# Kernel tuning notes

Hardware: AMD Instinct MI355X
Metric: run time of the kernel (lower is better)

The kernel has to match this reference:

```python
import jax, jax.numpy as jnp
import numpy as np

NUM_DAYOFWEEK, NUM_TIME, NUM_MONTH, NUM_DAY = 7, 24, 12, 31
NUM_DESTINATION = 100000
NUM_FACTOR = 128
NUM_DIM = NUM_FACTOR // 4  # 32
N = 1048576


def setup_inputs() -> dict:
    key = jax.random.key(0)
    ks = jax.random.split(key, 10)
    std = 0.1
    return {
        "dayofweek": jax.random.randint(ks[0], (N,), 0, NUM_DAYOFWEEK),
        "time": jax.random.randint(ks[1], (N,), 0, NUM_TIME),
        "month": jax.random.randint(ks[2], (N,), 0, NUM_MONTH),
        "day": jax.random.randint(ks[3], (N,), 0, NUM_DAY),
        "destination": jax.random.randint(ks[4], (N,), 0, NUM_DESTINATION),
        "W_dayofweek": std * jax.random.normal(ks[5], (NUM_DAYOFWEEK, NUM_DIM), dtype=jnp.float32),
        "W_time": std * jax.random.normal(ks[6], (NUM_TIME, NUM_DIM), dtype=jnp.float32),
        "W_month": std * jax.random.normal(ks[7], (NUM_MONTH, NUM_DIM), dtype=jnp.float32),
        "W_day": std * jax.random.normal(ks[8], (NUM_DAY, NUM_DIM), dtype=jnp.float32),
        "W_item": std * jax.random.normal(ks[9], (NUM_DESTINATION, NUM_FACTOR), dtype=jnp.float32),
    }


def reference(dayofweek, time, month, day, destination,
              W_dayofweek, W_time, W_month, W_day, W_item) -> jnp.ndarray:
    # Gather per-feature embeddings and concat into user vector [N, num_factor]
    user = jnp.concatenate([
        W_dayofweek[dayofweek],  # [N, 32]
        W_time[time],            # [N, 32]
        W_month[month],          # [N, 32]
        W_day[day],              # [N, 32]
    ], axis=-1)
    item = W_item[destination]   # [N, 128]
    # Original: diagonal(mm(user, item.T)) == rowwise dot product; compute it directly.
    return jnp.sum(user * item, axis=-1)  # [N]
```

## Files before the change

### kernel.cpp

```cpp
#include <hip/hip_runtime.h>


typedef unsigned long long u64;

constexpr int NDIM = 32;
constexpr int SZ_DOW = 7 * NDIM, SZ_TIM = 24 * NDIM, SZ_MON = 12 * NDIM, SZ_DAY = 31 * NDIM;
constexpr int B_DOW = 0;
constexpr int B_TIM = B_DOW + SZ_DOW;
constexpr int B_MON = B_TIM + SZ_TIM;
constexpr int B_DAY = B_MON + SZ_MON;
constexpr int TAB_TOT = B_DAY + SZ_DAY;

constexpr int NB     = 32;
constexpr int DDIV   = 3125;
constexpr int SLICES = 256;
constexpr int SPB    = 4096;
constexpr int BIN_T  = 1024;
constexpr int IPT    = SPB / BIN_T;

__device__ __forceinline__ unsigned short f2bf(float f) {
    const unsigned u = __float_as_uint(f);
    return (unsigned short)((u + 0x7FFFu + ((u >> 16) & 1u)) >> 16);
}

__device__ __forceinline__ float dot8bf(uint4 a, float4 u0, float4 u1) {
    float s;
    s  = __uint_as_float(a.x << 16)          * u0.x;
    s += __uint_as_float(a.x & 0xFFFF0000u)  * u0.y;
    s += __uint_as_float(a.y << 16)          * u0.z;
    s += __uint_as_float(a.y & 0xFFFF0000u)  * u0.w;
    s += __uint_as_float(a.z << 16)          * u1.x;
    s += __uint_as_float(a.z & 0xFFFF0000u)  * u1.y;
    s += __uint_as_float(a.w << 16)          * u1.z;
    s += __uint_as_float(a.w & 0xFFFF0000u)  * u1.w;
    return s;
}

__device__ __forceinline__ void load_tab(float* tab, const float* Wdow, const float* Wtim,
                                         const float* Wmon, const float* Wday, int nthr) {
    const int t = threadIdx.x;
    for (int i = t; i < SZ_DOW; i += nthr) tab[B_DOW + i] = Wdow[i];
    for (int i = t; i < SZ_TIM; i += nthr) tab[B_TIM + i] = Wtim[i];
    for (int i = t; i < SZ_MON; i += nthr) tab[B_MON + i] = Wmon[i];
    for (int i = t; i < SZ_DAY; i += nthr) tab[B_DAY + i] = Wday[i];
}

__global__ __launch_bounds__(BIN_T)
void prep_kernel(const int* __restrict__ dow, const int* __restrict__ tim,
                 const int* __restrict__ mon, const int* __restrict__ day,
                 const int* __restrict__ dest,
                 int* __restrict__ cntG, int* __restrict__ lbaseG,
                 u64* __restrict__ payload, int n,
                 const float* __restrict__ Witem, unsigned short* __restrict__ Wb,
                 int witem_elems)
{
    __shared__ u64 stage[SPB];
    __shared__ int hist[NB], lbase[NB], cursor[NB];

    const int t = threadIdx.x, b = blockIdx.x;
    const int g0 = b * SPB;
    const int rem = n - g0;
    const int len = rem < SPB ? rem : SPB;

    int dreg[IPT], pkreg[IPT];
#pragma unroll
    for (int i = 0; i < IPT; i++) {
        const int k = i * BIN_T + t;
        if (k < len) {
            const int idx = g0 + k;
            dreg[i]  = dest[idx];
            pkreg[i] = dow[idx] | (tim[idx] << 3) | (mon[idx] << 8) | (day[idx] << 12);
        } else { dreg[i] = -1; pkreg[i] = 0; }
    }

    if (Wb) {
        const int nf4   = witem_elems >> 2;
        const int chunk = (nf4 + SLICES - 1) / SLICES;
        const int c0    = b * chunk;
        const int c1    = min(c0 + chunk, nf4);
        const float4* src = (const float4*)Witem;
        ushort4* dst = (ushort4*)Wb;
        for (int i = c0 + t; i < c1; i += BIN_T) {
            const float4 v = src[i];
            ushort4 o;
            o.x = f2bf(v.x); o.y = f2bf(v.y); o.z = f2bf(v.z); o.w = f2bf(v.w);
            dst[i] = o;
        }
    }

    if (t < NB) hist[t] = 0;
    __syncthreads();
#pragma unroll
    for (int i = 0; i < IPT; i++)
        if (dreg[i] >= 0) atomicAdd(&hist[dreg[i] / DDIV], 1);
    __syncthreads();
    if (t == 0) {
        int run = 0;
        for (int q = 0; q < NB; q++) { lbase[q] = run; run += hist[q]; }
    }
    __syncthreads();
    if (t < NB) { cursor[t] = lbase[t]; cntG[b * NB + t] = hist[t]; lbaseG[b * NB + t] = lbase[t]; }
    __syncthreads();
#pragma unroll
    for (int i = 0; i < IPT; i++) {
        const int k = i * BIN_T + t;
        if (k < len) {
            const int j = atomicAdd(&cursor[dreg[i] / DDIV], 1);
            stage[j] = (u64)(unsigned)(g0 + k)
                     | ((u64)(unsigned)dreg[i]  << 20)
                     | ((u64)(unsigned)pkreg[i] << 37);
        }
    }
    __syncthreads();
#pragma unroll
    for (int i = 0; i < IPT; i++) {
        const int k = i * BIN_T + t;
        if (k < len) payload[g0 + k] = stage[k];
    }
}

__global__ __launch_bounds__(256, 8)
void mf_main_bf16(const u64* __restrict__ payload,
                  const float* __restrict__ Wdow, const float* __restrict__ Wtim,
                  const float* __restrict__ Wmon, const float* __restrict__ Wday,
                  const unsigned short* __restrict__ Wb,
                  const int* __restrict__ cntG, const int* __restrict__ lbaseG,
                  float* __restrict__ out)
{
    __shared__ float tab[TAB_TOT];
    load_tab(tab, Wdow, Wtim, Wmon, Wday, 256);
    __syncthreads();

    const int tid = threadIdx.x;
    const int sub = tid & 63;
    const int wv  = tid >> 6;
    const int g   = sub >> 3;
    const int l8  = sub & 7;
    const int jt   = l8 >> 1;
    const int half = (l8 & 1) * 16;
    const int tbj  = (jt == 0) ? B_DOW : (jt == 1) ? B_TIM : (jt == 2) ? B_MON : B_DAY;
    const int shj  = (jt == 0) ? 37    : (jt == 1) ? 40    : (jt == 2) ? 45    : 49;
    const int mkj  = (jt == 0) ? 7     : (jt == 1) ? 31    : (jt == 2) ? 15    : 31;

    const int x = blockIdx.x & 7;
    const int s = blockIdx.x >> 3;

    for (int p = 0; p < 4; p++) {
        const int q  = x + 8 * p;
        const int L  = cntG[s * NB + q];
        const int st = s * SPB + lbaseG[s * NB + q];

        int i = wv * 16;
        u64 p0 = (i + g < L)     ? payload[st + i + g]     : 0ull;
        u64 p1 = (i + 8 + g < L) ? payload[st + i + 8 + g] : 0ull;

        for (; i < L; i += 64) {
            const bool v0 = (i + g) < L, v1 = (i + 8 + g) < L;
            const u64 c0 = p0, c1 = p1;
            const int ni = i + 64;
            p0 = (ni + g < L)     ? payload[st + ni + g]     : 0ull;
            p1 = (ni + 8 + g < L) ? payload[st + ni + 8 + g] : 0ull;

            const int d0 = (int)((c0 >> 20) & 0x1FFFFull);
            const int d1 = (int)((c1 >> 20) & 0x1FFFFull);

            const uint4* r0 = (const uint4*)(Wb + (long)d0 * 128 + (l8 << 4));
            const uint4* r1 = (const uint4*)(Wb + (long)d1 * 128 + (l8 << 4));
            const uint4 A0 = r0[0], B0 = r0[1];
            const uint4 A1 = r1[0], B1 = r1[1];

            const int ix0 = (int)((c0 >> shj) & (u64)mkj);
            const int ix1 = (int)((c1 >> shj) & (u64)mkj);
            const float* u0p = &tab[tbj + ix0 * NDIM + half];
            const float* u1p = &tab[tbj + ix1 * NDIM + half];
            const float4 u00 = *(const float4*)(u0p);
            const float4 u01 = *(const float4*)(u0p + 4);
            const float4 u02 = *(const float4*)(u0p + 8);
            const float4 u03 = *(const float4*)(u0p + 12);
            const float4 u10 = *(const float4*)(u1p);
            const float4 u11 = *(const float4*)(u1p + 4);
            const float4 u12 = *(const float4*)(u1p + 8);
            const float4 u13 = *(const float4*)(u1p + 12);

            float a0 = dot8bf(A0, u00, u01) + dot8bf(B0, u02, u03);
            float a1 = dot8bf(A1, u10, u11) + dot8bf(B1, u12, u13);

            a0 += __shfl_xor(a0, 1);  a1 += __shfl_xor(a1, 1);
            a0 += __shfl_xor(a0, 2);  a1 += __shfl_xor(a1, 2);
            a0 += __shfl_xor(a0, 4);  a1 += __shfl_xor(a1, 4);

            if (l8 == 0) {
                if (v0) out[(int)(c0 & 0xFFFFFull)] = a0;
                if (v1) out[(int)(c1 & 0xFFFFFull)] = a1;
            }
        }
    }
}

__global__ __launch_bounds__(256, 8)
void mf_main_f32(const u64* __restrict__ payload,
                 const float* __restrict__ Wdow, const float* __restrict__ Wtim,
                 const float* __restrict__ Wmon, const float* __restrict__ Wday,
                 const float* __restrict__ Witem,
                 const int* __restrict__ cntG, const int* __restrict__ lbaseG,
                 float* __restrict__ out)
{
    __shared__ float tab[TAB_TOT];
    load_tab(tab, Wdow, Wtim, Wmon, Wday, 256);
    __syncthreads();
    const int tid = threadIdx.x;
    const int sub = tid & 63;
    const int wv  = tid >> 6;
    const int g   = sub >> 3;
    const int l8  = sub & 7;
    const int col = l8 * 4;
    const int tb[4] = {B_DOW, B_TIM, B_MON, B_DAY};
    const int sh[4] = {37, 40, 45, 49};
    const int mk[4] = {7, 31, 15, 31};
    const int x = blockIdx.x & 7;
    const int s = blockIdx.x >> 3;
    for (int p = 0; p < 4; p++) {
        const int q  = x + 8 * p;
        const int L  = cntG[s * NB + q];
        const int st = s * SPB + lbaseG[s * NB + q];
        for (int i = wv * 16; i < L; i += 64) {
            const int i0 = i + g, i1 = i + 8 + g;
            const bool v0 = i0 < L, v1 = i1 < L;
            const u64 p0 = v0 ? payload[st + i0] : 0ull;
            const u64 p1 = v1 ? payload[st + i1] : 0ull;
            const int d0 = (int)((p0 >> 20) & 0x1FFFFull);
            const int d1 = (int)((p1 >> 20) & 0x1FFFFull);
            const float* r0 = Witem + (long)d0 * 128 + col;
            const float* r1 = Witem + (long)d1 * 128 + col;
            float4 it0[4], it1[4], us0[4], us1[4];
#pragma unroll
            for (int j = 0; j < 4; j++) it0[j] = *reinterpret_cast<const float4*>(r0 + j * NDIM);
#pragma unroll
            for (int j = 0; j < 4; j++) it1[j] = *reinterpret_cast<const float4*>(r1 + j * NDIM);
#pragma unroll
            for (int j = 0; j < 4; j++) {
                const int idx = (int)((p0 >> sh[j]) & (u64)mk[j]);
                us0[j] = *reinterpret_cast<const float4*>(&tab[tb[j] + idx * NDIM + col]);
            }
#pragma unroll
            for (int j = 0; j < 4; j++) {
                const int idx = (int)((p1 >> sh[j]) & (u64)mk[j]);
                us1[j] = *reinterpret_cast<const float4*>(&tab[tb[j] + idx * NDIM + col]);
            }
            float a0 = 0.f, a1 = 0.f;
#pragma unroll
            for (int j = 0; j < 4; j++) {
                a0 += it0[j].x * us0[j].x + it0[j].y * us0[j].y
                    + it0[j].z * us0[j].z + it0[j].w * us0[j].w;
                a1 += it1[j].x * us1[j].x + it1[j].y * us1[j].y
                    + it1[j].z * us1[j].z + it1[j].w * us1[j].w;
            }
            a0 += __shfl_xor(a0, 1);  a1 += __shfl_xor(a1, 1);
            a0 += __shfl_xor(a0, 2);  a1 += __shfl_xor(a1, 2);
            a0 += __shfl_xor(a0, 4);  a1 += __shfl_xor(a1, 4);
            if (l8 == 0) {
                if (v0) out[(int)(p0 & 0xFFFFFull)] = a0;
                if (v1) out[(int)(p1 & 0xFFFFFull)] = a1;
            }
        }
    }
}

__global__ __launch_bounds__(256, 8)
void mf_dot_kernel(const int* __restrict__ dow, const int* __restrict__ tim,
                   const int* __restrict__ mon, const int* __restrict__ day,
                   const int* __restrict__ dest,
                   const float* __restrict__ Wdow, const float* __restrict__ Wtim,
                   const float* __restrict__ Wmon, const float* __restrict__ Wday,
                   const float* __restrict__ Witem,
                   float* __restrict__ out, int n_samples)
{
    __shared__ float tab[TAB_TOT];
    load_tab(tab, Wdow, Wtim, Wmon, Wday, 256);
    __syncthreads();
    const int tid = threadIdx.x;
    const int lane = tid & 63, sub = lane & 31, wave = tid >> 6, half = lane >> 5;
    const int t = sub >> 3, dofs = (sub & 7) * 4;
    const int* idxp  = (t == 0) ? dow   : (t == 1) ? tim   : (t == 2) ? mon   : day;
    const int  tbase = (t == 0) ? B_DOW : (t == 1) ? B_TIM : (t == 2) ? B_MON : B_DAY;
    long n = (long)blockIdx.x * 8 + wave * 2 + half;
    const long stride = (long)gridDim.x * 8;
    for (; n < n_samples; n += stride) {
        const int idx = idxp[n];
        const int ds  = dest[n];
        const float4 u  = *reinterpret_cast<const float4*>(&tab[tbase + idx * NDIM + dofs]);
        const float4 it = *reinterpret_cast<const float4*>(&Witem[(long)ds * 128 + sub * 4]);
        float r = u.x * it.x + u.y * it.y + u.z * it.z + u.w * it.w;
        r += __shfl_xor(r, 16); r += __shfl_xor(r, 8); r += __shfl_xor(r, 4);
        r += __shfl_xor(r, 2);  r += __shfl_xor(r, 1);
        if (sub == 0) out[n] = r;
    }
}

extern "C" void kernel_launch(void* const* d_in, const int* in_sizes, int n_in,
                              void* d_out, int out_size, void* d_ws, size_t ws_size,
                              hipStream_t stream)
{
    const int*   dow   = (const int*)d_in[0];
    const int*   tim   = (const int*)d_in[1];
    const int*   mon   = (const int*)d_in[2];
    const int*   day   = (const int*)d_in[3];
    const int*   dest  = (const int*)d_in[4];
    const float* Wdow  = (const float*)d_in[5];
    const float* Wtim  = (const float*)d_in[6];
    const float* Wmon  = (const float*)d_in[7];
    const float* Wday  = (const float*)d_in[8];
    const float* Witem = (const float*)d_in[9];
    float* out = (float*)d_out;

    const int n  = in_sizes[0];
    const int we = in_sizes[9];
    const int cap = SLICES * SPB;

    const size_t off_wb       = 64 * 1024;
    const size_t off_pay_full = (off_wb + (size_t)we * 2 + 255) & ~(size_t)255;
    const size_t need_full    = off_pay_full + (size_t)cap * 8;
    const size_t off_pay_mid  = 64 * 1024;
    const size_t need_mid     = off_pay_mid + (size_t)cap * 8;

    if ((size_t)ws_size < need_mid || n > cap) {
        hipLaunchKernelGGL(mf_dot_kernel, dim3(2048), dim3(256), 0, stream,
                           dow, tim, mon, day, dest,
                           Wdow, Wtim, Wmon, Wday, Witem, out, n);
        return;
    }

    const bool full = (size_t)ws_size >= need_full;

    int* cntG   = (int*)d_ws;
    int* lbaseG = (int*)((char*)d_ws + 32 * 1024);
    unsigned short* Wb = full ? (unsigned short*)((char*)d_ws + off_wb) : nullptr;
    u64* payload = (u64*)((char*)d_ws + (full ? off_pay_full : off_pay_mid));

    hipLaunchKernelGGL(prep_kernel, dim3(SLICES), dim3(BIN_T), 0, stream,
                       dow, tim, mon, day, dest, cntG, lbaseG, payload, n,
                       Witem, Wb, we);
    if (full)
        hipLaunchKernelGGL(mf_main_bf16, dim3(SLICES * 8), dim3(256), 0, stream,
                           payload, Wdow, Wtim, Wmon, Wday, Wb, cntG, lbaseG, out);
    else
        hipLaunchKernelGGL(mf_main_f32, dim3(SLICES * 8), dim3(256), 0, stream,
                           payload, Wdow, Wtim, Wmon, Wday, Witem, cntG, lbaseG, out);
}
```

Measured before the change: 150.9 us.

## Switch item and user tables to fp16 with packed fdot2 dot products

Converts the item table to fp16 instead of bf16 and stores the small user tables in shared memory as packed fp16, so the inner dot product uses v_dot2 (fdot2) instructions instead of unpacking to fp32 and doing scalar FMAs. The serial prefix scan in prep becomes a wave shuffle scan. Bin counts and bases are merged into one int2 array, and that array is loaded before the table staging. This cuts ALU work and LDS traffic per element. The cost is fp16 range and precision on the accumulation inputs.

```diff
diff --git a/kernel.cpp b/kernel.cpp
--- a/kernel.cpp
+++ b/kernel.cpp
@@ -2,6 +2,15 @@
 
 
 typedef unsigned long long u64;
+typedef unsigned int uint;
+typedef _Float16 half_t;
+typedef half_t h2 __attribute__((ext_vector_type(2)));
+
+#if __has_builtin(__builtin_amdgcn_fdot2)
+#define HAVE_FDOT2 1
+#else
+#define HAVE_FDOT2 0
+#endif
 
 constexpr int NDIM = 32;
 constexpr int SZ_DOW = 7 * NDIM, SZ_TIM = 24 * NDIM, SZ_MON = 12 * NDIM, SZ_DAY = 31 * NDIM;
@@ -18,22 +27,33 @@
 constexpr int BIN_T  = 1024;
 constexpr int IPT    = SPB / BIN_T;
 
-__device__ __forceinline__ unsigned short f2bf(float f) {
-    const unsigned u = __float_as_uint(f);
-    return (unsigned short)((u + 0x7FFFu + ((u >> 16) & 1u)) >> 16);
-}
-
-__device__ __forceinline__ float dot8bf(uint4 a, float4 u0, float4 u1) {
-    float s;
-    s  = __uint_as_float(a.x << 16)          * u0.x;
-    s += __uint_as_float(a.x & 0xFFFF0000u)  * u0.y;
-    s += __uint_as_float(a.y << 16)          * u0.z;
-    s += __uint_as_float(a.y & 0xFFFF0000u)  * u0.w;
-    s += __uint_as_float(a.z << 16)          * u1.x;
-    s += __uint_as_float(a.z & 0xFFFF0000u)  * u1.y;
-    s += __uint_as_float(a.w << 16)          * u1.z;
-    s += __uint_as_float(a.w & 0xFFFF0000u)  * u1.w;
-    return s;
+__device__ __forceinline__ unsigned short f2h(float f) {
+    return __builtin_bit_cast(unsigned short, (half_t)f);
+}
+
+__device__ __forceinline__ uint pack2h(float a, float b) {
+    return (uint)f2h(a) | ((uint)f2h(b) << 16);
+}
+
+__device__ __forceinline__ float dp2(uint a, uint b, float c) {
+#if HAVE_FDOT2
+    return __builtin_amdgcn_fdot2(__builtin_bit_cast(h2, a), __builtin_bit_cast(h2, b), c, false);
+#else
+    const h2 x = __builtin_bit_cast(h2, a), y = __builtin_bit_cast(h2, b);
+    return c + (float)x.x * (float)y.x + (float)x.y * (float)y.y;
+#endif
+}
+
+__device__ __forceinline__ float dot16h(uint4 a, uint4 b, uint4 ua, uint4 ub) {
+    float s0 = dp2(a.x, ua.x, 0.f);
+    float s1 = dp2(a.y, ua.y, 0.f);
+    s0 = dp2(a.z, ua.z, s0);
+    s1 = dp2(a.w, ua.w, s1);
+    s0 = dp2(b.x, ub.x, s0);
+    s1 = dp2(b.y, ub.y, s1);
+    s0 = dp2(b.z, ub.z, s0);
+    s1 = dp2(b.w, ub.w, s1);
+    return s0 + s1;
 }
 
 __device__ __forceinline__ void load_tab(float* tab, const float* Wdow, const float* Wtim,
@@ -45,17 +65,26 @@
     for (int i = t; i < SZ_DAY; i += nthr) tab[B_DAY + i] = Wday[i];
 }
 
+__device__ __forceinline__ void load_tabh(uint* th, const float* W, int base, int sz,
+                                          int t, int nthr) {
+    const float2* src = (const float2*)W;
+    for (int i = t; i < (sz >> 1); i += nthr) {
+        const float2 v = src[i];
+        th[(base >> 1) + i] = pack2h(v.x, v.y);
+    }
+}
+
 __global__ __launch_bounds__(BIN_T)
 void prep_kernel(const int* __restrict__ dow, const int* __restrict__ tim,
                  const int* __restrict__ mon, const int* __restrict__ day,
                  const int* __restrict__ dest,
-                 int* __restrict__ cntG, int* __restrict__ lbaseG,
+                 int2* __restrict__ clG,
                  u64* __restrict__ payload, int n,
-                 const float* __restrict__ Witem, unsigned short* __restrict__ Wb,
+                 const float* __restrict__ Witem, unsigned short* __restrict__ Wh,
                  int witem_elems)
 {
     __shared__ u64 stage[SPB];
-    __shared__ int hist[NB], lbase[NB], cursor[NB];
+    __shared__ int hist[NB], cursor[NB];
 
     const int t = threadIdx.x, b = blockIdx.x;
     const int g0 = b * SPB;
@@ -73,17 +102,17 @@
         } else { dreg[i] = -1; pkreg[i] = 0; }
     }
 
-    if (Wb) {
+    if (Wh) {
         const int nf4   = witem_elems >> 2;
         const int chunk = (nf4 + SLICES - 1) / SLICES;
         const int c0    = b * chunk;
         const int c1    = min(c0 + chunk, nf4);
         const float4* src = (const float4*)Witem;
-        ushort4* dst = (ushort4*)Wb;
+        ushort4* dst = (ushort4*)Wh;
         for (int i = c0 + t; i < c1; i += BIN_T) {
             const float4 v = src[i];
             ushort4 o;
-            o.x = f2bf(v.x); o.y = f2bf(v.y); o.z = f2bf(v.z); o.w = f2bf(v.w);
+            o.x = f2h(v.x); o.y = f2h(v.y); o.z = f2h(v.z); o.w = f2h(v.w);
             dst[i] = o;
         }
     }
@@ -94,12 +123,19 @@
     for (int i = 0; i < IPT; i++)
         if (dreg[i] >= 0) atomicAdd(&hist[dreg[i] / DDIV], 1);
     __syncthreads();
-    if (t == 0) {
-        int run = 0;
-        for (int q = 0; q < NB; q++) { lbase[q] = run; run += hist[q]; }
-    }
-    __syncthreads();
-    if (t < NB) { cursor[t] = lbase[t]; cntG[b * NB + t] = hist[t]; lbaseG[b * NB + t] = lbase[t]; }
+    if (t < 64) {
+        int v = (t < NB) ? hist[t] : 0;
+#pragma unroll
+        for (int d = 1; d < NB; d <<= 1) {
+            const int nv = __shfl_up(v, d);
+            if (t >= d) v += nv;
+        }
+        if (t < NB) {
+            const int base = v - hist[t];
+            cursor[t] = base;
+            clG[b * NB + t] = make_int2(hist[t], base);
+        }
+    }
     __syncthreads();
 #pragma unroll
     for (int i = 0; i < IPT; i++) {
@@ -120,18 +156,29 @@
 }
 
 __global__ __launch_bounds__(256, 8)
-void mf_main_bf16(const u64* __restrict__ payload,
-                  const float* __restrict__ Wdow, const float* __restrict__ Wtim,
-                  const float* __restrict__ Wmon, const float* __restrict__ Wday,
-                  const unsigned short* __restrict__ Wb,
-                  const int* __restrict__ cntG, const int* __restrict__ lbaseG,
-                  float* __restrict__ out)
-{
-    __shared__ float tab[TAB_TOT];
-    load_tab(tab, Wdow, Wtim, Wmon, Wday, 256);
-    __syncthreads();
+void mf_main_f16(const u64* __restrict__ payload,
+                 const float* __restrict__ Wdow, const float* __restrict__ Wtim,
+                 const float* __restrict__ Wmon, const float* __restrict__ Wday,
+                 const unsigned short* __restrict__ Wh,
+                 const int2* __restrict__ clG,
+                 float* __restrict__ out)
+{
+    __shared__ uint tabh[TAB_TOT / 2];
 
     const int tid = threadIdx.x;
+    const int x = blockIdx.x & 7;
+    const int s = blockIdx.x >> 3;
+
+    int2 cl[4];
+#pragma unroll
+    for (int p = 0; p < 4; p++) cl[p] = clG[s * NB + x + 8 * p];
+
+    load_tabh(tabh, Wdow, B_DOW, SZ_DOW, tid, 256);
+    load_tabh(tabh, Wtim, B_TIM, SZ_TIM, tid, 256);
+    load_tabh(tabh, Wmon, B_MON, SZ_MON, tid, 256);
+    load_tabh(tabh, Wday, B_DAY, SZ_DAY, tid, 256);
+    __syncthreads();
+
     const int sub = tid & 63;
     const int wv  = tid >> 6;
     const int g   = sub >> 3;
@@ -141,14 +188,11 @@
     const int tbj  = (jt == 0) ? B_DOW : (jt == 1) ? B_TIM : (jt == 2) ? B_MON : B_DAY;
     const int shj  = (jt == 0) ? 37    : (jt == 1) ? 40    : (jt == 2) ? 45    : 49;
     const int mkj  = (jt == 0) ? 7     : (jt == 1) ? 31    : (jt == 2) ? 15    : 31;
-
-    const int x = blockIdx.x & 7;
-    const int s = blockIdx.x >> 3;
+    const int tub  = (tbj + half) >> 1;
 
     for (int p = 0; p < 4; p++) {
-        const int q  = x + 8 * p;
-        const int L  = cntG[s * NB + q];
-        const int st = s * SPB + lbaseG[s * NB + q];
+        const int L  = cl[p].x;
+        const int st = s * SPB + cl[p].y;
 
         int i = wv * 16;
         u64 p0 = (i + g < L)     ? payload[st + i + g]     : 0ull;
@@ -164,26 +208,20 @@
             const int d0 = (int)((c0 >> 20) & 0x1FFFFull);
             const int d1 = (int)((c1 >> 20) & 0x1FFFFull);
 
-            const uint4* r0 = (const uint4*)(Wb + (long)d0 * 128 + (l8 << 4));
-            const uint4* r1 = (const uint4*)(Wb + (long)d1 * 128 + (l8 << 4));
+            const uint4* r0 = (const uint4*)(Wh + (long)d0 * 128 + (l8 << 4));
+            const uint4* r1 = (const uint4*)(Wh + (long)d1 * 128 + (l8 << 4));
             const uint4 A0 = r0[0], B0 = r0[1];
             const uint4 A1 = r1[0], B1 = r1[1];
 
             const int ix0 = (int)((c0 >> shj) & (u64)mkj);
             const int ix1 = (int)((c1 >> shj) & (u64)mkj);
-            const float* u0p = &tab[tbj + ix0 * NDIM + half];
-            const float* u1p = &tab[tbj + ix1 * NDIM + half];
-            const float4 u00 = *(const float4*)(u0p);
-            const float4 u01 = *(const float4*)(u0p + 4);
-            const float4 u02 = *(const float4*)(u0p + 8);
-            const float4 u03 = *(const float4*)(u0p + 12);
-            const float4 u10 = *(const float4*)(u1p);
-            const float4 u11 = *(const float4*)(u1p + 4);
-            const float4 u12 = *(const float4*)(u1p + 8);
-            const float4 u13 = *(const float4*)(u1p + 12);
-
-            float a0 = dot8bf(A0, u00, u01) + dot8bf(B0, u02, u03);
-            float a1 = dot8bf(A1, u10, u11) + dot8bf(B1, u12, u13);
+            const uint4* t0 = (const uint4*)&tabh[tub + ix0 * (NDIM / 2)];
+            const uint4* t1 = (const uint4*)&tabh[tub + ix1 * (NDIM / 2)];
+            const uint4 U00 = t0[0], U01 = t0[1];
+            const uint4 U10 = t1[0], U11 = t1[1];
+
+            float a0 = dot16h(A0, B0, U00, U01);
+            float a1 = dot16h(A1, B1, U10, U11);
 
             a0 += __shfl_xor(a0, 1);  a1 += __shfl_xor(a1, 1);
             a0 += __shfl_xor(a0, 2);  a1 += __shfl_xor(a1, 2);
@@ -202,13 +240,22 @@
                  const float* __restrict__ Wdow, const float* __restrict__ Wtim,
                  const float* __restrict__ Wmon, const float* __restrict__ Wday,
                  const float* __restrict__ Witem,
-                 const int* __restrict__ cntG, const int* __restrict__ lbaseG,
+                 const int2* __restrict__ clG,
                  float* __restrict__ out)
 {
     __shared__ float tab[TAB_TOT];
+
+    const int tid = threadIdx.x;
+    const int x = blockIdx.x & 7;
+    const int s = blockIdx.x >> 3;
+
+    int2 cl[4];
+#pragma unroll
+    for (int p = 0; p < 4; p++) cl[p] = clG[s * NB + x + 8 * p];
+
     load_tab(tab, Wdow, Wtim, Wmon, Wday, 256);
     __syncthreads();
-    const int tid = threadIdx.x;
+
     const int sub = tid & 63;
     const int wv  = tid >> 6;
     const int g   = sub >> 3;
@@ -217,12 +264,9 @@
     const int tb[4] = {B_DOW, B_TIM, B_MON, B_DAY};
     const int sh[4] = {37, 40, 45, 49};
     const int mk[4] = {7, 31, 15, 31};
-    const int x = blockIdx.x & 7;
-    const int s = blockIdx.x >> 3;
     for (int p = 0; p < 4; p++) {
-        const int q  = x + 8 * p;
-        const int L  = cntG[s * NB + q];
-        const int st = s * SPB + lbaseG[s * NB + q];
+        const int L  = cl[p].x;
+        const int st = s * SPB + cl[p].y;
         for (int i = wv * 16; i < L; i += 64) {
             const int i0 = i + g, i1 = i + 8 + g;
             const bool v0 = i0 < L, v1 = i1 < L;
@@ -317,8 +361,8 @@
     const int we = in_sizes[9];
     const int cap = SLICES * SPB;
 
-    const size_t off_wb       = 64 * 1024;
-    const size_t off_pay_full = (off_wb + (size_t)we * 2 + 255) & ~(size_t)255;
+    const size_t off_wh       = 64 * 1024;
+    const size_t off_pay_full = (off_wh + (size_t)we * 2 + 255) & ~(size_t)255;
     const size_t need_full    = off_pay_full + (size_t)cap * 8;
     const size_t off_pay_mid  = 64 * 1024;
     const size_t need_mid     = off_pay_mid + (size_t)cap * 8;
@@ -332,18 +376,17 @@
 
     const bool full = (size_t)ws_size >= need_full;
 
-    int* cntG   = (int*)d_ws;
-    int* lbaseG = (int*)((char*)d_ws + 32 * 1024);
-    unsigned short* Wb = full ? (unsigned short*)((char*)d_ws + off_wb) : nullptr;
+    int2* clG = (int2*)d_ws;
+    unsigned short* Wh = full ? (unsigned short*)((char*)d_ws + off_wh) : nullptr;
     u64* payload = (u64*)((char*)d_ws + (full ? off_pay_full : off_pay_mid));
 
     hipLaunchKernelGGL(prep_kernel, dim3(SLICES), dim3(BIN_T), 0, stream,
-                       dow, tim, mon, day, dest, cntG, lbaseG, payload, n,
-                       Witem, Wb, we);
+                       dow, tim, mon, day, dest, clG, payload, n,
+                       Witem, Wh, we);
     if (full)
-        hipLaunchKernelGGL(mf_main_bf16, dim3(SLICES * 8), dim3(256), 0, stream,
-                           payload, Wdow, Wtim, Wmon, Wday, Wb, cntG, lbaseG, out);
+        hipLaunchKernelGGL(mf_main_f16, dim3(SLICES * 8), dim3(256), 0, stream,
+                           payload, Wdow, Wtim, Wmon, Wday, Wh, clG, out);
     else
         hipLaunchKernelGGL(mf_main_f32, dim3(SLICES * 8), dim3(256), 0, stream,
-                           payload, Wdow, Wtim, Wmon, Wday, Witem, cntG, lbaseG, out);
-}
+                           payload, Wdow, Wtim, Wmon, Wday, Witem, clG, out);
+}
```

Result: faster. 147.5 us (-2.3%).
